# Kernel optimization log

Measured on AMD Instinct MI355X. Metric: run time of the kernel, lower is better.

## Reference

```python
import jax, jax.numpy as jnp
import numpy as np

GAMMA = 0.1
TAU = 0.01
N, M, K = 256, 512, 512


def setup_inputs() -> dict:
    key = jax.random.key(0)
    ks = jax.random.split(key, 10)
    nn2 = N * N
    return {
        "I": jax.random.normal(ks[0], (K, 1), dtype=jnp.float32),
        "x": jax.random.normal(ks[1], (N, 1), dtype=jnp.float32),
        "W": jax.random.normal(ks[2], (N, N), dtype=jnp.float32),
        "z": jax.random.normal(ks[3], (M, 1), dtype=jnp.float32),
        "C": jax.random.normal(ks[4], (nn2,), dtype=jnp.float32) / np.float32(np.sqrt(nn2)),
        "D": jax.random.normal(ks[5], (nn2, M), dtype=jnp.float32) / np.float32(np.sqrt(nn2)),
        "F": jax.random.normal(ks[6], (M,), dtype=jnp.float32) / np.float32(np.sqrt(M)),
        "H": jax.random.normal(ks[7], (M, nn2), dtype=jnp.float32) / np.float32(np.sqrt(M)),
        "W_in_1": jax.random.uniform(ks[8], (N, K), dtype=jnp.float32, minval=-1.0 / np.sqrt(K), maxval=1.0 / np.sqrt(K)),
        "W_in_2": jax.random.uniform(ks[9], (M, K), dtype=jnp.float32, minval=-1.0 / np.sqrt(K), maxval=1.0 / np.sqrt(K)),
    }


def reference(I, x, W, z, C, D, F, H, W_in_1, W_in_2):
    n = x.shape[0]
    # neuron state update: x' = (1-g)x + g*W@phi(x) + W_in_1@I
    phi_x = jax.nn.sigmoid(x)                       # (n,1)
    x_new = (1.0 - GAMMA) * x + GAMMA * (W @ phi_x) + W_in_1 @ I
    # Phi(x') = vec(phi(x') phi(x')^T), row-major -> (n*n, 1)
    phi_xn = jax.nn.sigmoid(x_new)                  # (n,1)
    Phi = (phi_xn * phi_xn.T).reshape(-1, 1)        # (n*n,1) outer product
    psi_z = jnp.tanh(z)                             # (m,1)
    # diag(C)@Phi is an elementwise multiply; D@psi(z) is the big GEMV
    W_new = (1.0 - GAMMA) * W + GAMMA * (C[:, None] * Phi + D @ psi_z).reshape(n, n)
    # astrocyte update: diag(F)@psi(z) elementwise; H@Phi big GEMV
    z_new = (1.0 - GAMMA * TAU) * z + GAMMA * TAU * (
        F[:, None] * psi_z + H @ Phi + W_in_2 @ I
    )
    return (x_new, W_new, z_new)
```

## Files before the change

### kernel.cpp

```cpp
#include <hip/hip_runtime.h>
#include <math.h>

#define GAMMA 0.1f
#define TAU   0.01f
#define NN    256
#define MM    512
#define KK    512

__device__ __forceinline__ float sigmoidf(float v) {
    return 1.0f / (1.0f + __expf(-v));
}
__device__ __forceinline__ float4 sigmoid4(float4 v) {
    return make_float4(sigmoidf(v.x), sigmoidf(v.y), sigmoidf(v.z), sigmoidf(v.w));
}
__device__ __forceinline__ float dot4(float4 a, float4 b) {
    return a.x * b.x + a.y * b.y + a.z * b.z + a.w * b.w;
}

__global__ __launch_bounds__(256) void k_state(
    const float* __restrict__ I, const float* __restrict__ x,
    const float* __restrict__ W, const float* __restrict__ z,
    const float* __restrict__ Win1,
    float* __restrict__ out, float* __restrict__ ws)
{
    const int b = blockIdx.x, t = threadIdx.x;
    if (b < 16) {
        const int wave = t >> 6, lane = t & 63;
        const int row0 = b * 16 + wave * 4;
        float4 xv = ((const float4*)x)[lane];
        float4 i0 = ((const float4*)I)[lane];
        float4 i1 = ((const float4*)I)[64 + lane];
        const float4* Wr = (const float4*)(W + row0 * NN);
        float4 w0 = Wr[lane], w1 = Wr[lane + 64], w2 = Wr[lane + 128], w3 = Wr[lane + 192];
        const float4* A = (const float4*)(Win1 + row0 * KK);
        float4 a0 = A[lane],       c0 = A[lane + 64];
        float4 a1 = A[lane + 128], c1 = A[lane + 192];
        float4 a2 = A[lane + 256], c2 = A[lane + 320];
        float4 a3 = A[lane + 384], c3 = A[lane + 448];
        float4 xo = ((const float4*)x)[row0 >> 2];

        float4 ph = sigmoid4(xv);
        float s0 = GAMMA * dot4(w0, ph) + dot4(a0, i0) + dot4(c0, i1);
        float s1 = GAMMA * dot4(w1, ph) + dot4(a1, i0) + dot4(c1, i1);
        float s2 = GAMMA * dot4(w2, ph) + dot4(a2, i0) + dot4(c2, i1);
        float s3 = GAMMA * dot4(w3, ph) + dot4(a3, i0) + dot4(c3, i1);
#pragma unroll
        for (int m = 32; m; m >>= 1) {
            s0 += __shfl_xor(s0, m, 64);
            s1 += __shfl_xor(s1, m, 64);
            s2 += __shfl_xor(s2, m, 64);
            s3 += __shfl_xor(s3, m, 64);
        }
        if (lane == 0) {
            float4 xn;
            xn.x = (1.0f - GAMMA) * xo.x + s0;
            xn.y = (1.0f - GAMMA) * xo.y + s1;
            xn.z = (1.0f - GAMMA) * xo.z + s2;
            xn.w = (1.0f - GAMMA) * xo.w + s3;
            ((float4*)out)[row0 >> 2] = xn;
            ((float4*)ws)[row0 >> 2] = sigmoid4(xn);
        }
    } else {
        const int idx = (b - 16) * 256 + t;
        ws[NN + idx] = tanhf(z[idx]);
    }
}

__global__ __launch_bounds__(256) void k_big(
    const float* __restrict__ W, const float* __restrict__ Cv,
    const float* __restrict__ D, const float* __restrict__ F,
    const float* __restrict__ H, const float* __restrict__ Win2,
    const float* __restrict__ I, const float* __restrict__ z,
    const float* __restrict__ ws, float* __restrict__ out)
{
    __shared__ float sm[768];
    __shared__ float red[4];
    const int b = blockIdx.x, t = threadIdx.x;

    if (b < MM) {
        if (t < 64) ((float4*)sm)[t] = ((const float4*)ws)[t];
        float wi = Win2[(size_t)b * KK + t] * I[t]
                 + Win2[(size_t)b * KK + 256 + t] * I[256 + t];
        __syncthreads();
        const float4* H4 = (const float4*)(H + (size_t)b * (NN * NN));
        const float4 pj = ((const float4*)sm)[t & 63];
        const int wv4 = t >> 6;
        float acc = wi;
#pragma unroll 16
        for (int q = 0; q < 64; ++q) {
            float4 h = H4[t + 256 * q];
            acc += sm[wv4 + 4 * q] * dot4(h, pj);
        }
#pragma unroll
        for (int m = 32; m; m >>= 1) acc += __shfl_xor(acc, m, 64);
        if ((t & 63) == 0) red[t >> 6] = acc;
        __syncthreads();
        if (t == 0) {
            const float gt = GAMMA * TAU;
            float tot = red[0] + red[1] + red[2] + red[3];
            float zn = (1.0f - gt) * z[b] + gt * (F[b] * ws[NN + b] + tot);
            out[NN + NN * NN + b] = zn;
        }
    } else {
        if (t < 128)      ((float4*)sm)[t] = ((const float4*)(ws + NN))[t];
        else if (t < 192) ((float4*)sm)[t] = ((const float4*)ws)[t - 128];
        __syncthreads();
        const int wave = t >> 6, lane = t & 63;
        const float4 z0 = ((const float4*)sm)[lane];
        const float4 z1 = ((const float4*)sm)[64 + lane];
        const int row0 = (b - MM) * 32 + wave * 8;
        const float4* R = (const float4*)(D + (size_t)row0 * MM);
        float4 pA = R[lane],       qA = R[lane + 64];
        float4 pB = R[lane + 128], qB = R[lane + 192];
        float4 pC = R[lane + 256], qC = R[lane + 320];
        float4 pD = R[lane + 384], qD = R[lane + 448];
        float4 pE = R[lane + 512], qE = R[lane + 576];
        float4 pF = R[lane + 640], qF = R[lane + 704];
        float4 pG = R[lane + 768], qG = R[lane + 832];
        float4 pH = R[lane + 896], qH = R[lane + 960];
        float4 w0 = ((const float4*)W)[row0 >> 2],  w1 = ((const float4*)W)[(row0 >> 2) + 1];
        float4 c0 = ((const float4*)Cv)[row0 >> 2], c1 = ((const float4*)Cv)[(row0 >> 2) + 1];

        float s0 = dot4(pA, z0) + dot4(qA, z1);
        float s1 = dot4(pB, z0) + dot4(qB, z1);
        float s2 = dot4(pC, z0) + dot4(qC, z1);
        float s3 = dot4(pD, z0) + dot4(qD, z1);
        float s4 = dot4(pE, z0) + dot4(qE, z1);
        float s5 = dot4(pF, z0) + dot4(qF, z1);
        float s6 = dot4(pG, z0) + dot4(qG, z1);
        float s7 = dot4(pH, z0) + dot4(qH, z1);
#pragma unroll
        for (int m = 32; m; m >>= 1) {
            s0 += __shfl_xor(s0, m, 64);
            s1 += __shfl_xor(s1, m, 64);
            s2 += __shfl_xor(s2, m, 64);
            s3 += __shfl_xor(s3, m, 64);
            s4 += __shfl_xor(s4, m, 64);
            s5 += __shfl_xor(s5, m, 64);
            s6 += __shfl_xor(s6, m, 64);
            s7 += __shfl_xor(s7, m, 64);
        }
        if (lane == 0) {
            const float phi_i = sm[512 + (row0 >> 8)];
            const float4* PJ = (const float4*)(sm + 512);
            float4 pj0 = PJ[(row0 & 255) >> 2], pj1 = PJ[((row0 & 255) >> 2) + 1];
            float4 r0, r1;
            r0.x = (1.0f - GAMMA) * w0.x + GAMMA * (c0.x * phi_i * pj0.x + s0);
            r0.y = (1.0f - GAMMA) * w0.y + GAMMA * (c0.y * phi_i * pj0.y + s1);
            r0.z = (1.0f - GAMMA) * w0.z + GAMMA * (c0.z * phi_i * pj0.z + s2);
            r0.w = (1.0f - GAMMA) * w0.w + GAMMA * (c0.w * phi_i * pj0.w + s3);
            r1.x = (1.0f - GAMMA) * w1.x + GAMMA * (c1.x * phi_i * pj1.x + s4);
            r1.y = (1.0f - GAMMA) * w1.y + GAMMA * (c1.y * phi_i * pj1.y + s5);
            r1.z = (1.0f - GAMMA) * w1.z + GAMMA * (c1.z * phi_i * pj1.z + s6);
            r1.w = (1.0f - GAMMA) * w1.w + GAMMA * (c1.w * phi_i * pj1.w + s7);
            ((float4*)(out + NN + row0))[0] = r0;
            ((float4*)(out + NN + row0))[1] = r1;
        }
    }
}

extern "C" void kernel_launch(void* const* d_in, const int* in_sizes, int n_in,
                              void* d_out, int out_size, void* d_ws, size_t ws_size,
                              hipStream_t stream) {
    const float* I    = (const float*)d_in[0];
    const float* x    = (const float*)d_in[1];
    const float* W    = (const float*)d_in[2];
    const float* z    = (const float*)d_in[3];
    const float* C    = (const float*)d_in[4];
    const float* D    = (const float*)d_in[5];
    const float* F    = (const float*)d_in[6];
    const float* H    = (const float*)d_in[7];
    const float* Win1 = (const float*)d_in[8];
    const float* Win2 = (const float*)d_in[9];
    float* out = (float*)d_out;
    float* ws  = (float*)d_ws;

    hipLaunchKernelGGL(k_state, dim3(18), dim3(256), 0, stream,
                       I, x, W, z, Win1, out, ws);
    hipLaunchKernelGGL(k_big, dim3(MM + (NN * NN) / 32), dim3(256), 0, stream,
                       W, C, D, F, H, Win2, I, z, ws, out);
}
```

Baseline: 297.0 us.

## Split fused GEMV kernel into separate H and D kernels with streaming loads

Splits the combined H/D GEMV kernel into two launches. The H GEMV now uses 1024-thread blocks with batched loads and four independent accumulators. The D GEMV uses non-temporal loads with double-buffered row prefetch, and each wave handles 16 rows with per-lane row outputs. The aim is more memory-level parallelism and less cache pollution while streaming the two large matrices. The cost is an extra kernel launch and the two phases no longer running concurrently.

```diff
diff --git a/kernel.cpp b/kernel.cpp
--- a/kernel.cpp
+++ b/kernel.cpp
@@ -7,6 +7,8 @@
 #define MM    512
 #define KK    512
 
+typedef float vf4 __attribute__((ext_vector_type(4)));
+
 __device__ __forceinline__ float sigmoidf(float v) {
     return 1.0f / (1.0f + __expf(-v));
 }
@@ -15,6 +17,10 @@
 }
 __device__ __forceinline__ float dot4(float4 a, float4 b) {
     return a.x * b.x + a.y * b.y + a.z * b.z + a.w * b.w;
+}
+__device__ __forceinline__ float4 ntload4(const float4* p) {
+    vf4 v = __builtin_nontemporal_load((const vf4*)p);
+    return make_float4(v.x, v.y, v.z, v.w);
 }
 
 __global__ __launch_bounds__(256) void k_state(
@@ -66,96 +72,103 @@
     }
 }
 
-__global__ __launch_bounds__(256) void k_big(
-    const float* __restrict__ W, const float* __restrict__ Cv,
-    const float* __restrict__ D, const float* __restrict__ F,
+__global__ __launch_bounds__(1024, 4) void k_H(
     const float* __restrict__ H, const float* __restrict__ Win2,
     const float* __restrict__ I, const float* __restrict__ z,
-    const float* __restrict__ ws, float* __restrict__ out)
+    const float* __restrict__ F, const float* __restrict__ ws,
+    float* __restrict__ out)
+{
+    __shared__ float sm[256];
+    __shared__ float red[16];
+    const int b = blockIdx.x, t = threadIdx.x;
+    if (t < 64) ((float4*)sm)[t] = ((const float4*)ws)[t];
+    float wi = 0.0f;
+    if (t < KK) wi = Win2[(size_t)b * KK + t] * I[t];
+    __syncthreads();
+    const float4* H4 = (const float4*)(H + (size_t)b * (NN * NN));
+    const float4 pj = ((const float4*)sm)[t & 63];
+    const int i0 = t >> 6;
+    float a0 = wi, a1 = 0.0f, a2 = 0.0f, a3 = 0.0f;
+#pragma unroll
+    for (int qq = 0; qq < 2; ++qq) {
+        float4 h[8];
+        float  pi[8];
+#pragma unroll
+        for (int u = 0; u < 8; ++u) {
+            const int q = qq * 8 + u;
+            h[u]  = H4[t + 1024 * q];
+            pi[u] = sm[i0 + 16 * q];
+        }
+#pragma unroll
+        for (int u = 0; u < 8; ++u) {
+            const float term = pi[u] * dot4(h[u], pj);
+            if      ((u & 3) == 0) a0 += term;
+            else if ((u & 3) == 1) a1 += term;
+            else if ((u & 3) == 2) a2 += term;
+            else                   a3 += term;
+        }
+    }
+    float acc = (a0 + a1) + (a2 + a3);
+#pragma unroll
+    for (int m = 32; m; m >>= 1) acc += __shfl_xor(acc, m, 64);
+    if ((t & 63) == 0) red[t >> 6] = acc;
+    __syncthreads();
+    if (t < 64) {
+        float v = (t < 16) ? red[t] : 0.0f;
+#pragma unroll
+        for (int m = 8; m; m >>= 1) v += __shfl_xor(v, m, 64);
+        if (t == 0) {
+            const float gt = GAMMA * TAU;
+            float zn = (1.0f - gt) * z[b] + gt * (F[b] * ws[NN + b] + v);
+            out[NN + NN * NN + b] = zn;
+        }
+    }
+}
+
+__global__ __launch_bounds__(256) void k_D(
+    const float* __restrict__ W, const float* __restrict__ Cv,
+    const float* __restrict__ D, const float* __restrict__ ws,
+    float* __restrict__ out)
 {
     __shared__ float sm[768];
-    __shared__ float red[4];
-    const int b = blockIdx.x, t = threadIdx.x;
+    const int t = threadIdx.x;
+    if (t < 128)      ((float4*)sm)[t] = ((const float4*)(ws + NN))[t];
+    else if (t < 192) ((float4*)sm)[t] = ((const float4*)ws)[t - 128];
+    __syncthreads();
+    const int wave = t >> 6, lane = t & 63;
+    const float4 z0 = ((const float4*)sm)[lane];
+    const float4 z1 = ((const float4*)sm)[64 + lane];
+    const int row0 = blockIdx.x * 64 + wave * 16;
+    const float4* R = (const float4*)(D + (size_t)row0 * MM);
 
-    if (b < MM) {
-        if (t < 64) ((float4*)sm)[t] = ((const float4*)ws)[t];
-        float wi = Win2[(size_t)b * KK + t] * I[t]
-                 + Win2[(size_t)b * KK + 256 + t] * I[256 + t];
-        __syncthreads();
-        const float4* H4 = (const float4*)(H + (size_t)b * (NN * NN));
-        const float4 pj = ((const float4*)sm)[t & 63];
-        const int wv4 = t >> 6;
-        float acc = wi;
-#pragma unroll 16
-        for (int q = 0; q < 64; ++q) {
-            float4 h = H4[t + 256 * q];
-            acc += sm[wv4 + 4 * q] * dot4(h, pj);
+    float wrow = 0.0f, crow = 0.0f, pjrow = 0.0f;
+    if (lane < 16) {
+        wrow  = W[row0 + lane];
+        crow  = Cv[row0 + lane];
+        pjrow = sm[512 + (row0 & 255) + lane];
+    }
+    const float pi = sm[512 + (row0 >> 8)];
+
+    float4 fa0 = ntload4(&R[lane]),        fb0 = ntload4(&R[lane + 64]);
+    float4 fa1 = ntload4(&R[lane + 128]),  fb1 = ntload4(&R[lane + 192]);
+    float keep = 0.0f;
+#pragma unroll
+    for (int r = 0; r < 16; ++r) {
+        float4 ca, cb;
+        if (r & 1) { ca = fa1; cb = fb1; } else { ca = fa0; cb = fb0; }
+        if (r + 2 < 16) {
+            const float4* Rn = R + (r + 2) * 128;
+            if (r & 1) { fa1 = ntload4(&Rn[lane]); fb1 = ntload4(&Rn[lane + 64]); }
+            else       { fa0 = ntload4(&Rn[lane]); fb0 = ntload4(&Rn[lane + 64]); }
         }
+        float s = dot4(ca, z0) + dot4(cb, z1);
 #pragma unroll
-        for (int m = 32; m; m >>= 1) acc += __shfl_xor(acc, m, 64);
-        if ((t & 63) == 0) red[t >> 6] = acc;
-        __syncthreads();
-        if (t == 0) {
-            const float gt = GAMMA * TAU;
-            float tot = red[0] + red[1] + red[2] + red[3];
-            float zn = (1.0f - gt) * z[b] + gt * (F[b] * ws[NN + b] + tot);
-            out[NN + NN * NN + b] = zn;
-        }
-    } else {
-        if (t < 128)      ((float4*)sm)[t] = ((const float4*)(ws + NN))[t];
-        else if (t < 192) ((float4*)sm)[t] = ((const float4*)ws)[t - 128];
-        __syncthreads();
-        const int wave = t >> 6, lane = t & 63;
-        const float4 z0 = ((const float4*)sm)[lane];
-        const float4 z1 = ((const float4*)sm)[64 + lane];
-        const int row0 = (b - MM) * 32 + wave * 8;
-        const float4* R = (const float4*)(D + (size_t)row0 * MM);
-        float4 pA = R[lane],       qA = R[lane + 64];
-        float4 pB = R[lane + 128], qB = R[lane + 192];
-        float4 pC = R[lane + 256], qC = R[lane + 320];
-        float4 pD = R[lane + 384], qD = R[lane + 448];
-        float4 pE = R[lane + 512], qE = R[lane + 576];
-        float4 pF = R[lane + 640], qF = R[lane + 704];
-        float4 pG = R[lane + 768], qG = R[lane + 832];
-        float4 pH = R[lane + 896], qH = R[lane + 960];
-        float4 w0 = ((const float4*)W)[row0 >> 2],  w1 = ((const float4*)W)[(row0 >> 2) + 1];
-        float4 c0 = ((const float4*)Cv)[row0 >> 2], c1 = ((const float4*)Cv)[(row0 >> 2) + 1];
-
-        float s0 = dot4(pA, z0) + dot4(qA, z1);
-        float s1 = dot4(pB, z0) + dot4(qB, z1);
-        float s2 = dot4(pC, z0) + dot4(qC, z1);
-        float s3 = dot4(pD, z0) + dot4(qD, z1);
-        float s4 = dot4(pE, z0) + dot4(qE, z1);
-        float s5 = dot4(pF, z0) + dot4(qF, z1);
-        float s6 = dot4(pG, z0) + dot4(qG, z1);
-        float s7 = dot4(pH, z0) + dot4(qH, z1);
-#pragma unroll
-        for (int m = 32; m; m >>= 1) {
-            s0 += __shfl_xor(s0, m, 64);
-            s1 += __shfl_xor(s1, m, 64);
-            s2 += __shfl_xor(s2, m, 64);
-            s3 += __shfl_xor(s3, m, 64);
-            s4 += __shfl_xor(s4, m, 64);
-            s5 += __shfl_xor(s5, m, 64);
-            s6 += __shfl_xor(s6, m, 64);
-            s7 += __shfl_xor(s7, m, 64);
-        }
-        if (lane == 0) {
-            const float phi_i = sm[512 + (row0 >> 8)];
-            const float4* PJ = (const float4*)(sm + 512);
-            float4 pj0 = PJ[(row0 & 255) >> 2], pj1 = PJ[((row0 & 255) >> 2) + 1];
-            float4 r0, r1;
-            r0.x = (1.0f - GAMMA) * w0.x + GAMMA * (c0.x * phi_i * pj0.x + s0);
-            r0.y = (1.0f - GAMMA) * w0.y + GAMMA * (c0.y * phi_i * pj0.y + s1);
-            r0.z = (1.0f - GAMMA) * w0.z + GAMMA * (c0.z * phi_i * pj0.z + s2);
-            r0.w = (1.0f - GAMMA) * w0.w + GAMMA * (c0.w * phi_i * pj0.w + s3);
-            r1.x = (1.0f - GAMMA) * w1.x + GAMMA * (c1.x * phi_i * pj1.x + s4);
-            r1.y = (1.0f - GAMMA) * w1.y + GAMMA * (c1.y * phi_i * pj1.y + s5);
-            r1.z = (1.0f - GAMMA) * w1.z + GAMMA * (c1.z * phi_i * pj1.z + s6);
-            r1.w = (1.0f - GAMMA) * w1.w + GAMMA * (c1.w * phi_i * pj1.w + s7);
-            ((float4*)(out + NN + row0))[0] = r0;
-            ((float4*)(out + NN + row0))[1] = r1;
-        }
+        for (int m = 32; m; m >>= 1) s += __shfl_xor(s, m, 64);
+        if (lane == r) keep = s;
+    }
+    if (lane < 16) {
+        float wn = (1.0f - GAMMA) * wrow + GAMMA * (crow * pi * pjrow + keep);
+        out[NN + row0 + lane] = wn;
     }
 }
 
@@ -177,6 +190,8 @@
 
     hipLaunchKernelGGL(k_state, dim3(18), dim3(256), 0, stream,
                        I, x, W, z, Win1, out, ws);
-    hipLaunchKernelGGL(k_big, dim3(MM + (NN * NN) / 32), dim3(256), 0, stream,
-                       W, C, D, F, H, Win2, I, z, ws, out);
+    hipLaunchKernelGGL(k_H, dim3(MM), dim3(1024), 0, stream,
+                       H, Win2, I, z, F, ws, out);
+    hipLaunchKernelGGL(k_D, dim3((NN * NN) / 64), dim3(256), 0, stream,
+                       W, C, D, ws, out);
 }
```

After: 284.0 us. 1.05x faster.
